# Kernel optimization log

Measured on AMD Instinct MI355X. Metric: run time of the kernel, lower is better.

Reference implementation:

```python
import jax, jax.numpy as jnp
import numpy as np

NUM_REL = 6
EMBED_DIM = 128
B, N = 8, 1024


def _relation_type(dx, dy):
    # Faithful to _get_relation_type's if/elif chain (order matters).
    return jnp.select(
        [dy > 0.5,
         dy < -0.5,
         dx < -0.5,
         dx > 0.5,
         (jnp.abs(dx) < 0.3) & (jnp.abs(dy) < 0.3)],
        [0, 1, 2, 3, 4],
        5,
    )


def setup_inputs() -> dict:
    key = jax.random.key(0)
    k1, k2, k3, k4 = jax.random.split(key, 4)
    symbols = jax.random.normal(k1, (B, N, EMBED_DIM), dtype=jnp.float32)
    positions = jax.random.normal(k2, (B, N, 2), dtype=jnp.float32)
    # 6 Linear(embed_dim, embed_dim) layers, stacked: W [6, D, D] (torch layout: y = x @ W.T + b)
    bound = 1.0 / np.sqrt(EMBED_DIM)
    W = jax.random.uniform(k3, (NUM_REL, EMBED_DIM, EMBED_DIM), dtype=jnp.float32,
                           minval=-bound, maxval=bound)
    b = jax.random.uniform(k4, (NUM_REL, EMBED_DIM), dtype=jnp.float32,
                           minval=-bound, maxval=bound)
    return {"symbols": symbols, "positions": positions, "W": W, "b": b}


def reference(symbols, positions, W, b):
    Bn, Nn, D = symbols.shape
    # dx[b,i,j] = pos[b,j,0] - pos[b,i,0]; dy likewise (source i -> target j)
    dx = positions[:, None, :, 0] - positions[:, :, None, 0]  # [B, i, j]
    dy = positions[:, None, :, 1] - positions[:, :, None, 1]
    rel = _relation_type(dx, dy)  # [B, i, j] in {0..5}

    # Per-type transform of every source symbol: T[r,b,i,:] = symbols[b,i] @ W[r].T + b[r]
    T = jnp.einsum('bid,red->rbie', symbols, W) + b[:, None, None, :]  # [6, B, N, D]

    # One-hot relation mask with i != j excluded; scatter-add into targets j.
    not_diag = ~jnp.eye(Nn, dtype=bool)  # [i, j]
    mask = (rel[None] == jnp.arange(NUM_REL)[:, None, None, None]) & not_diag  # [6, B, i, j]
    agg = jnp.einsum('rbij,rbie->bje', mask.astype(symbols.dtype), T)  # [B, N, D]
    return symbols + agg
```

## Files before the change

kernel.cpp:

```cpp
#include <hip/hip_runtime.h>
#include <stdint.h>


typedef __attribute__((ext_vector_type(8))) short bf16x8;
typedef __attribute__((ext_vector_type(4))) float f32x4;
union U4B { uint4 u; bf16x8 b; };

#if defined(__has_builtin)
#  if __has_builtin(__builtin_amdgcn_mul_u24)
#    define OH_MUL24 1
#  endif
#endif

__device__ __forceinline__ uint16_t f2bf(float f) {
    union { float f; uint32_t u; } v; v.f = f;
    uint32_t u = v.u;
    uint32_t r = (u + 0x7FFFu + ((u >> 16) & 1u)) >> 16;
    return (uint16_t)r;
}

__global__ __launch_bounds__(256)
void prep_kernel(const float* __restrict__ X, const float* __restrict__ W,
                 uint16_t* __restrict__ symT, uint16_t* __restrict__ WtB) {
    const int blk = blockIdx.x, tid = threadIdx.x;
    if (blk < 256) {
        __shared__ float T[64 * 65];
        const int b = blk & 7, z = blk >> 3, it = z & 15, et = z >> 4;
        const int i0 = it * 64, e0 = et * 64;
        const float4* Xf = (const float4*)X;
#pragma unroll
        for (int s = 0; s < 4; ++s) {
            int il = s * 16 + (tid >> 4), e4 = tid & 15;
            float4 v = Xf[((size_t)b << 15) + (size_t)((i0 + il) << 5) + (e0 >> 2) + e4];
            T[il * 65 + e4 * 4 + 0] = v.x;
            T[il * 65 + e4 * 4 + 1] = v.y;
            T[il * 65 + e4 * 4 + 2] = v.z;
            T[il * 65 + e4 * 4 + 3] = v.w;
        }
        __syncthreads();
#pragma unroll
        for (int s = 0; s < 4; ++s) {
            int el = s * 16 + (tid >> 4), il4 = tid & 15;
            uint16_t h0 = f2bf(T[(il4 * 4 + 0) * 65 + el]);
            uint16_t h1 = f2bf(T[(il4 * 4 + 1) * 65 + el]);
            uint16_t h2 = f2bf(T[(il4 * 4 + 2) * 65 + el]);
            uint16_t h3 = f2bf(T[(il4 * 4 + 3) * 65 + el]);
            uint2 pk = { (uint32_t)h0 | ((uint32_t)h1 << 16),
                         (uint32_t)h2 | ((uint32_t)h3 << 16) };
            *(uint2*)&symT[((size_t)b << 17) + ((size_t)(e0 + el) << 10) + i0 + il4 * 4] = pk;
        }
    } else {
        int g = (blk - 256) * 256 + tid;
        float4 v = ((const float4*)W)[g];
        int r = g >> 12, rem = g & 4095, ep = rem >> 5, e4 = rem & 31;
        int kb = r * 4 + (e4 >> 3);
        int kc = (e4 & 7) * 4;
        uint16_t h0 = f2bf(v.x), h1 = f2bf(v.y), h2 = f2bf(v.z), h3 = f2bf(v.w);
        uint2 pk = { (uint32_t)h0 | ((uint32_t)h1 << 16),
                     (uint32_t)h2 | ((uint32_t)h3 << 16) };
        *(uint2*)&WtB[((size_t)(kb * 128 + ep)) * 32 + kc] = pk;
    }
}

#define RELDW 258
#define SP 776

__global__ __launch_bounds__(512)
__attribute__((amdgpu_waves_per_eu(2, 4)))
void fused_kernel(const float* __restrict__ sym, const float* __restrict__ pos,
                  const uint16_t* __restrict__ symT, const uint16_t* __restrict__ WtB,
                  const float* __restrict__ bias, float* __restrict__ out) {
    __shared__ __align__(16) char smem[72192];
    float2*   posS    = (float2*)smem;
    uint16_t* symTS   = (uint16_t*)smem;
    uint16_t* SA      = (uint16_t*)smem;
    uint32_t* rel32   = (uint32_t*)(smem + 34816);
    float*    partial = (float*)(smem + 34816);
    uint16_t* cntP    = (uint16_t*)(smem + 34816 + 16512);
    float*    cntF    = (float*)(smem + 68608);
    float*    biasS   = (float*)(smem + 69120);

    const int blk = blockIdx.x;
    const int b = blk & 7, jt = blk >> 3, j0 = jt * 16;
    const int tid = threadIdx.x;
    const int w = tid >> 6, lane = tid & 63, m = lane & 15, q = lane >> 4;

    const uint16_t* symTb = symT + ((size_t)b << 17);

    uint4 pf[4];
#pragma unroll
    for (int s = 0; s < 4; ++s) {
        int f = s * 512 + tid, e = f >> 4, seg = f & 15;
        pf[s] = *(const uint4*)&symTb[(e << 10) + seg * 8];
    }

    const float2* pos2 = (const float2*)pos + ((size_t)b << 10);
    posS[tid] = pos2[tid];
    posS[tid + 512] = pos2[tid + 512];
    biasS[tid] = bias[tid];
    if (tid < 256) biasS[tid + 512] = bias[tid + 512];
    __syncthreads();

    {
        const int mm = tid & 15, grp = tid >> 4;
        const int j = j0 + mm;
        const float2 pj = posS[j];
        uint32_t a0 = 0, a1 = 0, a2 = 0, a3 = 0, a4 = 0, a5 = 0;
        uint32_t* dst = &rel32[mm * RELDW + grp * 8];
#pragma unroll
        for (int s = 0; s < 8; ++s) {
            uint32_t word = 0;
#pragma unroll
            for (int qq = 0; qq < 4; ++qq) {
                int i = grp * 32 + s * 4 + qq;
                float2 pi = posS[i];
                float dx = pj.x - pi.x, dy = pj.y - pi.y;
                int r = (dy > 0.5f) ? 0
                      : (dy < -0.5f) ? 1
                      : (dx < -0.5f) ? 2
                      : (dx > 0.5f)  ? 3
                      : (fabsf(dx) < 0.3f && fabsf(dy) < 0.3f) ? 4
                      : 5;
                uint32_t oh = (i == j) ? 0u : (1u << r);
                word |= oh << (8 * qq);
            }
            dst[s] = word;
            a0 += word & 0x01010101u;
            a1 += (word >> 1) & 0x01010101u;
            a2 += (word >> 2) & 0x01010101u;
            a3 += (word >> 3) & 0x01010101u;
            a4 += (word >> 4) & 0x01010101u;
            a5 += (word >> 5) & 0x01010101u;
        }
        uint16_t* cp = &cntP[(mm * 32 + grp) * 6];
        cp[0] = (uint16_t)((a0 * 0x01010101u) >> 24);
        cp[1] = (uint16_t)((a1 * 0x01010101u) >> 24);
        cp[2] = (uint16_t)((a2 * 0x01010101u) >> 24);
        cp[3] = (uint16_t)((a3 * 0x01010101u) >> 24);
        cp[4] = (uint16_t)((a4 * 0x01010101u) >> 24);
        cp[5] = (uint16_t)((a5 * 0x01010101u) >> 24);
    }
    __syncthreads();
    if (tid < 96) {
        int j2 = tid / 6, r2 = tid - j2 * 6;
        int s = 0;
#pragma unroll
        for (int g = 0; g < 32; ++g) s += cntP[(j2 * 32 + g) * 6 + r2];
        cntF[j2 * 8 + r2] = (float)s;
    }

    f32x4 acc[6];
#pragma unroll
    for (int r = 0; r < 6; ++r) acc[r] = (f32x4){0.f, 0.f, 0.f, 0.f};

    for (int c = 0; c < 8; ++c) {
#pragma unroll
        for (int s = 0; s < 4; ++s) {
            int f = s * 512 + tid, e = f >> 4, seg = f & 15;
            *(uint4*)&symTS[e * 136 + seg * 8] = pf[s];
        }
        __syncthreads();
        if (c < 7) {
#pragma unroll
            for (int s = 0; s < 4; ++s) {
                int f = s * 512 + tid, e = f >> 4, seg = f & 15;
                pf[s] = *(const uint4*)&symTb[(e << 10) + (c + 1) * 128 + seg * 8];
            }
        }
        const uint16_t* bt = &symTS[(w * 16 + m) * 136];
        const uint32_t* cr = &rel32[m * RELDW + c * 32 + q * 2];
#pragma unroll
        for (int ks = 0; ks < 4; ++ks) {
            U4B bfr;
            bfr.u = *(const uint4*)(bt + ks * 32 + q * 8);
            uint2 cw = *(const uint2*)(cr + ks * 8);
            uint32_t hx01 = __builtin_amdgcn_perm(cw.x, cw.x, 0x01010000u) & 0x00FF00FFu;
            uint32_t hx23 = __builtin_amdgcn_perm(cw.x, cw.x, 0x03030202u) & 0x00FF00FFu;
            uint32_t hy01 = __builtin_amdgcn_perm(cw.y, cw.y, 0x01010000u) & 0x00FF00FFu;
            uint32_t hy23 = __builtin_amdgcn_perm(cw.y, cw.y, 0x03030202u) & 0x00FF00FFu;
#pragma unroll
            for (int r = 0; r < 6; ++r) {
                const uint32_t rm = 0x00010001u << r;
                U4B a;
#ifdef OH_MUL24
                const uint32_t mc = 0x3F80u >> r;
                a.u.x = (uint32_t)__builtin_amdgcn_mul_u24((int)(hx01 & rm), (int)mc);
                a.u.y = (uint32_t)__builtin_amdgcn_mul_u24((int)(hx23 & rm), (int)mc);
                a.u.z = (uint32_t)__builtin_amdgcn_mul_u24((int)(hy01 & rm), (int)mc);
                a.u.w = (uint32_t)__builtin_amdgcn_mul_u24((int)(hy23 & rm), (int)mc);
#else
                uint32_t g;
                g = hx01 & rm; a.u.x = (g << (14 - r)) - (g << (7 - r));
                g = hx23 & rm; a.u.y = (g << (14 - r)) - (g << (7 - r));
                g = hy01 & rm; a.u.z = (g << (14 - r)) - (g << (7 - r));
                g = hy23 & rm; a.u.w = (g << (14 - r)) - (g << (7 - r));
#endif
                acc[r] = __builtin_amdgcn_mfma_f32_16x16x32_bf16(a.b, bfr.b, acc[r], 0, 0, 0);
            }
        }
        __syncthreads();
    }

#pragma unroll
    for (int r = 0; r < 6; ++r)
#pragma unroll
        for (int reg = 0; reg < 4; ++reg)
            SA[(q * 4 + reg) * SP + r * 128 + w * 16 + m] = f2bf(acc[r][reg]);
    __syncthreads();

    {
        const int g = w >> 1, h = w & 1;
        f32x4 c2[4];
#pragma unroll
        for (int nf = 0; nf < 4; ++nf) c2[nf] = (f32x4){0.f, 0.f, 0.f, 0.f};
#pragma unroll
        for (int kf = 0; kf < 6; ++kf) {
            U4B af;
            af.u = *(const uint4*)&SA[m * SP + g * 192 + kf * 32 + q * 8];
            const int kb = g * 6 + kf;
#pragma unroll
            for (int nf = 0; nf < 4; ++nf) {
                U4B bw;
                bw.u = *(const uint4*)&WtB[((size_t)(kb * 128 + h * 64 + nf * 16 + m)) * 32 + q * 8];
                c2[nf] = __builtin_amdgcn_mfma_f32_16x16x32_bf16(af.b, bw.b, c2[nf], 0, 0, 0);
            }
        }
#pragma unroll
        for (int nf = 0; nf < 4; ++nf)
#pragma unroll
            for (int reg = 0; reg < 4; ++reg)
                partial[g * 2112 + (q * 4 + reg) * 132 + h * 64 + nf * 16 + m] = c2[nf][reg];
    }
    __syncthreads();

    {
        const int j = tid >> 5, e0 = (tid & 31) * 4;
        float4 a4 = {0.f, 0.f, 0.f, 0.f};
#pragma unroll
        for (int g4 = 0; g4 < 4; ++g4) {
            float4 u = *(const float4*)&partial[g4 * 2112 + j * 132 + e0];
            a4.x += u.x; a4.y += u.y; a4.z += u.z; a4.w += u.w;
        }
#pragma unroll
        for (int r = 0; r < 6; ++r) {
            float cf = cntF[j * 8 + r];
            float4 bb = *(const float4*)&biasS[r * 128 + e0];
            a4.x += cf * bb.x; a4.y += cf * bb.y; a4.z += cf * bb.z; a4.w += cf * bb.w;
        }
        size_t o = ((size_t)(b * 1024 + j0 + j) << 7) + e0;
        float4 s0 = *(const float4*)&sym[o];
        float4 o0 = { s0.x + a4.x, s0.y + a4.y, s0.z + a4.z, s0.w + a4.w };
        *(float4*)&out[o] = o0;
    }
}

extern "C" void kernel_launch(void* const* d_in, const int* in_sizes, int n_in,
                              void* d_out, int out_size, void* d_ws, size_t ws_size,
                              hipStream_t stream) {
    const float* symbols   = (const float*)d_in[0];
    const float* positions = (const float*)d_in[1];
    const float* W         = (const float*)d_in[2];
    const float* bias      = (const float*)d_in[3];
    float* out             = (float*)d_out;

    char* ws = (char*)d_ws;
    uint16_t* symT = (uint16_t*)ws;
    uint16_t* WtB  = (uint16_t*)(ws + 2097152);

    prep_kernel<<<352, 256, 0, stream>>>(symbols, W, symT, WtB);
    fused_kernel<<<512, 512, 0, stream>>>(symbols, positions, symT, WtB, bias, out);
}
```

Baseline: 112.7 us.

## Double-buffer symT chunks via direct global-to-LDS loads with XOR swizzle

Replaces the register-staged prefetch of symT chunks with global_load_lds into two alternating LDS buffers, using an XOR swizzle in place of padding to avoid bank conflicts. The per-relation counts are moved out of the relation-building phase into the epilogue, computed with a wave shuffle reduction, and bias is read directly from global memory. The waves_per_eu attribute is dropped and LDS usage rises to 80KB. The aim is to overlap chunk loads with MFMA work and drop a sync and the register round-trip. The cost is a larger LDS footprint, which may limit occupancy, and the diff shows no explicit wait on the async LDS loads before they are consumed.

```diff
diff --git a/kernel.cpp b/kernel.cpp
--- a/kernel.cpp
+++ b/kernel.cpp
@@ -7,6 +7,9 @@
 union U4B { uint4 u; bf16x8 b; };
 
 #if defined(__has_builtin)
+#  if __has_builtin(__builtin_amdgcn_global_load_lds)
+#    define HAVE_GLL 1
+#  endif
 #  if __has_builtin(__builtin_amdgcn_mul_u24)
 #    define OH_MUL24 1
 #  endif
@@ -62,23 +65,18 @@
     }
 }
 
-#define RELDW 258
 #define SP 776
 
 __global__ __launch_bounds__(512)
-__attribute__((amdgpu_waves_per_eu(2, 4)))
 void fused_kernel(const float* __restrict__ sym, const float* __restrict__ pos,
                   const uint16_t* __restrict__ symT, const uint16_t* __restrict__ WtB,
                   const float* __restrict__ bias, float* __restrict__ out) {
-    __shared__ __align__(16) char smem[72192];
-    float2*   posS    = (float2*)smem;
+    __shared__ __align__(16) char smem[81920];
     uint16_t* symTS   = (uint16_t*)smem;
+    float2*   posS    = (float2*)(smem + 32768);
     uint16_t* SA      = (uint16_t*)smem;
-    uint32_t* rel32   = (uint32_t*)(smem + 34816);
-    float*    partial = (float*)(smem + 34816);
-    uint16_t* cntP    = (uint16_t*)(smem + 34816 + 16512);
-    float*    cntF    = (float*)(smem + 68608);
-    float*    biasS   = (float*)(smem + 69120);
+    float*    partial = (float*)(smem + 24832);
+    uint32_t* rel32   = (uint32_t*)(smem + 65536);
 
     const int blk = blockIdx.x;
     const int b = blk & 7, jt = blk >> 3, j0 = jt * 16;
@@ -87,26 +85,47 @@
 
     const uint16_t* symTb = symT + ((size_t)b << 17);
 
-    uint4 pf[4];
+    int goff[4];
 #pragma unroll
     for (int s = 0; s < 4; ++s) {
-        int f = s * 512 + tid, e = f >> 4, seg = f & 15;
-        pf[s] = *(const uint4*)&symTb[(e << 10) + seg * 8];
-    }
+        int c16 = s * 512 + tid;
+        int e = c16 >> 4, sg = (c16 & 15) ^ (e & 15);
+        goff[s] = (e << 10) + sg * 8;
+    }
+    const int lwb = w * 1024;
+
+    auto issue_chunk = [&](int cidx, int bufsel) {
+#ifdef HAVE_GLL
+#pragma unroll
+        for (int s = 0; s < 4; ++s) {
+            const uint16_t* gp = symTb + goff[s] + cidx * 128;
+            char* lp = smem + bufsel * 32768 + s * 8192 + lwb;
+            typedef const __attribute__((address_space(1))) uint32_t gu32;
+            typedef __attribute__((address_space(3))) uint32_t lu32;
+            __builtin_amdgcn_global_load_lds((gu32*)gp, (lu32*)lp, 16, 0, 0);
+        }
+#else
+#pragma unroll
+        for (int s = 0; s < 4; ++s) {
+            uint4 v = *(const uint4*)(symTb + goff[s] + cidx * 128);
+            *(uint4*)(smem + bufsel * 32768 + (s * 512 + tid) * 16) = v;
+        }
+#endif
+    };
+
+    issue_chunk(0, 0);
 
     const float2* pos2 = (const float2*)pos + ((size_t)b << 10);
     posS[tid] = pos2[tid];
     posS[tid + 512] = pos2[tid + 512];
-    biasS[tid] = bias[tid];
-    if (tid < 256) biasS[tid + 512] = bias[tid + 512];
     __syncthreads();
 
     {
         const int mm = tid & 15, grp = tid >> 4;
         const int j = j0 + mm;
         const float2 pj = posS[j];
-        uint32_t a0 = 0, a1 = 0, a2 = 0, a3 = 0, a4 = 0, a5 = 0;
-        uint32_t* dst = &rel32[mm * RELDW + grp * 8];
+        uint32_t* dst = &rel32[mm * 256];
+        const int sw = mm * 2;
 #pragma unroll
         for (int s = 0; s < 8; ++s) {
             uint32_t word = 0;
@@ -124,56 +143,28 @@
                 uint32_t oh = (i == j) ? 0u : (1u << r);
                 word |= oh << (8 * qq);
             }
-            dst[s] = word;
-            a0 += word & 0x01010101u;
-            a1 += (word >> 1) & 0x01010101u;
-            a2 += (word >> 2) & 0x01010101u;
-            a3 += (word >> 3) & 0x01010101u;
-            a4 += (word >> 4) & 0x01010101u;
-            a5 += (word >> 5) & 0x01010101u;
-        }
-        uint16_t* cp = &cntP[(mm * 32 + grp) * 6];
-        cp[0] = (uint16_t)((a0 * 0x01010101u) >> 24);
-        cp[1] = (uint16_t)((a1 * 0x01010101u) >> 24);
-        cp[2] = (uint16_t)((a2 * 0x01010101u) >> 24);
-        cp[3] = (uint16_t)((a3 * 0x01010101u) >> 24);
-        cp[4] = (uint16_t)((a4 * 0x01010101u) >> 24);
-        cp[5] = (uint16_t)((a5 * 0x01010101u) >> 24);
-    }
-    __syncthreads();
-    if (tid < 96) {
-        int j2 = tid / 6, r2 = tid - j2 * 6;
-        int s = 0;
-#pragma unroll
-        for (int g = 0; g < 32; ++g) s += cntP[(j2 * 32 + g) * 6 + r2];
-        cntF[j2 * 8 + r2] = (float)s;
-    }
+            dst[(grp * 8 + s) ^ sw] = word;
+        }
+    }
+    __syncthreads();
 
     f32x4 acc[6];
 #pragma unroll
     for (int r = 0; r < 6; ++r) acc[r] = (f32x4){0.f, 0.f, 0.f, 0.f};
 
+    const int E = w * 16 + m;
+    const int esw = E & 15;
+    const int csw = m * 2;
+
     for (int c = 0; c < 8; ++c) {
-#pragma unroll
-        for (int s = 0; s < 4; ++s) {
-            int f = s * 512 + tid, e = f >> 4, seg = f & 15;
-            *(uint4*)&symTS[e * 136 + seg * 8] = pf[s];
-        }
-        __syncthreads();
-        if (c < 7) {
-#pragma unroll
-            for (int s = 0; s < 4; ++s) {
-                int f = s * 512 + tid, e = f >> 4, seg = f & 15;
-                pf[s] = *(const uint4*)&symTb[(e << 10) + (c + 1) * 128 + seg * 8];
-            }
-        }
-        const uint16_t* bt = &symTS[(w * 16 + m) * 136];
-        const uint32_t* cr = &rel32[m * RELDW + c * 32 + q * 2];
+        if (c < 7) issue_chunk(c + 1, (c + 1) & 1);
+        const uint16_t* bt = symTS + ((c & 1) << 14) + E * 128;
+        const uint32_t* crow = &rel32[m * 256 + c * 32];
 #pragma unroll
         for (int ks = 0; ks < 4; ++ks) {
             U4B bfr;
-            bfr.u = *(const uint4*)(bt + ks * 32 + q * 8);
-            uint2 cw = *(const uint2*)(cr + ks * 8);
+            bfr.u = *(const uint4*)(bt + ((((ks << 2) + q) ^ esw) << 3));
+            uint2 cw = *(const uint2*)&crow[(((ks << 3) + (q << 1)) ^ csw)];
             uint32_t hx01 = __builtin_amdgcn_perm(cw.x, cw.x, 0x01010000u) & 0x00FF00FFu;
             uint32_t hx23 = __builtin_amdgcn_perm(cw.x, cw.x, 0x03030202u) & 0x00FF00FFu;
             uint32_t hy01 = __builtin_amdgcn_perm(cw.y, cw.y, 0x01010000u) & 0x00FF00FFu;
@@ -189,11 +180,11 @@
                 a.u.z = (uint32_t)__builtin_amdgcn_mul_u24((int)(hy01 & rm), (int)mc);
                 a.u.w = (uint32_t)__builtin_amdgcn_mul_u24((int)(hy23 & rm), (int)mc);
 #else
-                uint32_t g;
-                g = hx01 & rm; a.u.x = (g << (14 - r)) - (g << (7 - r));
-                g = hx23 & rm; a.u.y = (g << (14 - r)) - (g << (7 - r));
-                g = hy01 & rm; a.u.z = (g << (14 - r)) - (g << (7 - r));
-                g = hy23 & rm; a.u.w = (g << (14 - r)) - (g << (7 - r));
+                uint32_t g2;
+                g2 = hx01 & rm; a.u.x = (g2 << (14 - r)) - (g2 << (7 - r));
+                g2 = hx23 & rm; a.u.y = (g2 << (14 - r)) - (g2 << (7 - r));
+                g2 = hy01 & rm; a.u.z = (g2 << (14 - r)) - (g2 << (7 - r));
+                g2 = hy23 & rm; a.u.w = (g2 << (14 - r)) - (g2 << (7 - r));
 #endif
                 acc[r] = __builtin_amdgcn_mfma_f32_16x16x32_bf16(a.b, bfr.b, acc[r], 0, 0, 0);
             }
@@ -234,7 +225,29 @@
     __syncthreads();
 
     {
-        const int j = tid >> 5, e0 = (tid & 31) * 4;
+        const int j = tid >> 5, t = tid & 31, e0 = t << 2;
+        const uint32_t* row = &rel32[j * 256 + t * 8];
+        uint32_t s0 = 0, s1 = 0, s2 = 0, s3 = 0, s4 = 0, s5 = 0;
+#pragma unroll
+        for (int k = 0; k < 8; ++k) {
+            uint32_t wd = row[k];
+            s0 += wd & 0x01010101u;        s1 += (wd >> 1) & 0x01010101u;
+            s2 += (wd >> 2) & 0x01010101u; s3 += (wd >> 3) & 0x01010101u;
+            s4 += (wd >> 4) & 0x01010101u; s5 += (wd >> 5) & 0x01010101u;
+        }
+        int cnt[6];
+        cnt[0] = (int)((s0 * 0x01010101u) >> 24);
+        cnt[1] = (int)((s1 * 0x01010101u) >> 24);
+        cnt[2] = (int)((s2 * 0x01010101u) >> 24);
+        cnt[3] = (int)((s3 * 0x01010101u) >> 24);
+        cnt[4] = (int)((s4 * 0x01010101u) >> 24);
+        cnt[5] = (int)((s5 * 0x01010101u) >> 24);
+#pragma unroll
+        for (int off = 1; off < 32; off <<= 1)
+#pragma unroll
+            for (int r = 0; r < 6; ++r)
+                cnt[r] += __shfl_xor(cnt[r], off, 64);
+
         float4 a4 = {0.f, 0.f, 0.f, 0.f};
 #pragma unroll
         for (int g4 = 0; g4 < 4; ++g4) {
@@ -243,14 +256,14 @@
         }
 #pragma unroll
         for (int r = 0; r < 6; ++r) {
-            float cf = cntF[j * 8 + r];
-            float4 bb = *(const float4*)&biasS[r * 128 + e0];
+            float cf = (float)cnt[r];
+            float4 bb = *(const float4*)&bias[r * 128 + e0];
             a4.x += cf * bb.x; a4.y += cf * bb.y; a4.z += cf * bb.z; a4.w += cf * bb.w;
         }
         size_t o = ((size_t)(b * 1024 + j0 + j) << 7) + e0;
-        float4 s0 = *(const float4*)&sym[o];
-        float4 o0 = { s0.x + a4.x, s0.y + a4.y, s0.z + a4.z, s0.w + a4.w };
-        *(float4*)&out[o] = o0;
+        float4 sv = *(const float4*)&sym[o];
+        float4 ov = { sv.x + a4.x, sv.y + a4.y, sv.z + a4.z, sv.w + a4.w };
+        *(float4*)&out[o] = ov;
     }
 }
 
```

Result: faster. 92.21 us (-18.2%).
